# Performance work log

Hardware: AMD Instinct MI355X
Metric: run time of the kernel (lower is better)

The kernel has to match this reference:

```python
import jax, jax.numpy as jnp
import numpy as np

NUM_FEATURES = 256
HIDDEN = 32
ALPHA = 0.1
JITTER = 1e-4
QP_ITERS = 500  # fixed-iteration projected gradient solve of the nonneg-constrained QP
BATCH = 65536


def setup_inputs() -> dict:
    key = jax.random.key(0)
    ks = jax.random.split(key, 6)
    n, h = NUM_FEATURES, HIDDEN
    x = jax.random.normal(ks[0], (BATCH, n), jnp.float32)
    y = jax.random.normal(ks[1], (BATCH, 1), jnp.float32)
    # per-feature MLP params, stacked over the feature axis
    # first Linear has fan_in=1 -> torch init U(-1,1); second has fan_in=h -> U(-1/sqrt(h),1/sqrt(h))
    W1 = jax.random.uniform(ks[2], (n, h), jnp.float32, -1.0, 1.0)
    b1 = jax.random.uniform(ks[3], (n, h), jnp.float32, -1.0, 1.0)
    lim = 1.0 / np.sqrt(h)
    W2 = jax.random.uniform(ks[4], (n, h), jnp.float32, -lim, lim)
    b2 = jax.random.uniform(ks[5], (n,), jnp.float32, -lim, lim)
    return {"x": x, "y": y, "W1": W1, "b1": b1, "W2": W2, "b2": b2}


def _forward(x, y, W1, b1, W2, b2):
    B = x.shape[0]
    n = NUM_FEATURES
    # all per-feature 1->hidden->1 MLPs, batched over the feature axis
    hact = jnp.tanh(x[:, :, None] * W1[None, :, :] + b1[None, :, :])   # [B, n, hidden]
    Z = jnp.einsum('bnh,nh->bn', hact, W2) + b2                         # [B, n]
    Q = Z.T @ Z + JITTER * jnp.eye(n, dtype=Z.dtype)                    # Gram + jitter
    L = jnp.linalg.cholesky(Q)                                          # solver parameterization
    Qe = L @ L.T                                                        # == Q_stable; what the QP 'sees'
    p = ALPHA * B * jnp.ones(n, Z.dtype) - (Z.T @ y)[:, 0]
    # QP: min 0.5*lam^T Qe lam + p^T lam  s.t. lam >= 0 ; projected gradient, step = 1/lmax
    lmax = jnp.linalg.eigvalsh(jax.lax.stop_gradient(Qe))[-1]
    step = 1.0 / lmax

    def body(lam, _):
        lam = jnp.maximum(lam - step * (Qe @ lam + p), 0.0)
        return lam, None

    lam, _ = jax.lax.scan(body, jnp.zeros(n, Z.dtype), None, length=QP_ITERS)
    y_hat = Z @ lam                                                     # [B]
    return y_hat, lam


def reference(x, y, W1, b1, W2, b2):
    return _forward(x, y, W1, b1, W2, b2)
```

## Files before the change

### kernel.cpp

```cpp
#include <hip/hip_runtime.h>
#include <math.h>


#define NF 256
#define HID 32
#define BATCHN 65536
#define ALPHA_BF 6553.6f
#define JITTERF 1e-4f
#define QP_ITERS_N 500
#define K2C 2.8853900817779268f
#define XFIX 6.5f
#define INVX (1.0f / 6.5f)
#define NNODE 44

#if __has_builtin(__builtin_amdgcn_exp2f)
__device__ __forceinline__ float fexp2(float x) { return __builtin_amdgcn_exp2f(x); }
#else
__device__ __forceinline__ float fexp2(float x) { return exp2f(x); }
#endif
#if __has_builtin(__builtin_amdgcn_rcpf)
__device__ __forceinline__ float frcp(float x) { return __builtin_amdgcn_rcpf(x); }
#else
__device__ __forceinline__ float frcp(float x) { return 1.0f / x; }
#endif

__device__ __forceinline__ float zeval(const float* __restrict__ W1,
                                       const float* __restrict__ b1,
                                       const float* __restrict__ W2,
                                       const float* __restrict__ b2,
                                       int n, float xv)
{
  float acc = b2[n];
  for (int h = 0; h < HID; ++h) {
    float u  = fmaf(xv, W1[n * HID + h], b1[n * HID + h]);
    float th = fmaf(-2.f, frcp(fexp2(K2C * u) + 1.f), 1.f);
    acc = fmaf(W2[n * HID + h], th, acc);
  }
  return acc;
}

__global__ __launch_bounds__(256) void mcoeff_kernel(
    const float* __restrict__ y,
    const float* __restrict__ W1, const float* __restrict__ b1,
    const float* __restrict__ W2, float* __restrict__ wsf)
{
  const int t = threadIdx.x;
  if ((int)blockIdx.x < 64) {
    const int gi = blockIdx.x * 256 + t;
    if (gi == 0) wsf[1] = 0.f;
    if (gi == 2) wsf[2] = 0.f;
    float4 v = *reinterpret_cast<const float4*>(y + gi * 4);
    float s  = (v.x + v.y) + (v.z + v.w);
    float sa = (fabsf(v.x) + fabsf(v.y)) + (fabsf(v.z) + fabsf(v.w));
    #pragma unroll
    for (int m = 1; m < 64; m <<= 1) {
      s  += __shfl_xor(s, m);
      sa += __shfl_xor(sa, m);
    }
    __shared__ float ls[4], la[4];
    int w = t >> 6;
    if ((t & 63) == 0) { ls[w] = s; la[w] = sa; }
    __syncthreads();
    if (t == 0) {
      wsf[8  + blockIdx.x] = (ls[0] + ls[1]) + (ls[2] + ls[3]);
      wsf[72 + blockIdx.x] = (la[0] + la[1]) + (la[2] + la[3]);
    }
  } else {
    const int cb = blockIdx.x - 64;
    const int k  = cb >> 5;
    const int id = (cb & 31) * 256 + t;
    const int h  = t & 31;
    const int n  = id >> 5;
    const float aX  = W1[id] * XFIX;
    const float bb  = b1[id];
    const float w2v = W2[id];
    const float kf = (float)k;
    const float C1 = (float)(M_PI / (double)NNODE);
    float acc = 0.f;
    #pragma unroll 4
    for (int jn = 0; jn < NNODE; ++jn) {
      float ang = ((float)jn + 0.5f) * C1;
      float tj  = __cosf(ang);
      float u   = fmaf(aX, tj, bb);
      float f   = fmaf(-2.f, frcp(fexp2(K2C * u) + 1.f), 1.f);
      acc = fmaf(f, __cosf(kf * ang), acc);
    }
    const float ck = acc * ((k == 0) ? (1.0f / (float)NNODE)
                                     : (2.0f / (float)NNODE));
    float comb = w2v * ck;
    float cabs = fabsf(comb);
    float wabs = fabsf(w2v);
    #pragma unroll
    for (int m = 1; m < 32; m <<= 1) {
      comb += __shfl_xor(comb, m);
      cabs += __shfl_xor(cabs, m);
      wabs += __shfl_xor(wabs, m);
    }
    if (h == 0) {
      if (k <= 20) wsf[256 + k * 256 + n] = comb;
      else         wsf[5632 + (k - 21) * 256 + n] = cabs;
      if (k == 0)  wsf[11520 + n] = wabs;
    }
  }
}

#define STEP2(CK) { \
  float q0 = fmaf(d0, c0, -m0), q1 = fmaf(d1, c1, -m1); \
  a0 = fmaf(CK.x, q0, a0); a1 = fmaf(CK.y, q1, a1); \
  m0 = c0; c0 = q0; m1 = c1; c1 = q1; }

#define ROW2(XV, YV) { \
  mx = fmaxf(mx, fmaxf(fabsf((XV).x), fabsf((XV).y))); \
  float h0 = (XV).x * INVX, h1 = (XV).y * INVX; \
  float d0 = h0 + h0, d1 = h1 + h1; \
  float m0 = 1.f, m1 = 1.f, c0 = h0, c1 = h1; \
  float a0 = fmaf(C01.x, h0, C00.x), a1 = fmaf(C01.y, h1, C00.y); \
  STEP2(C02) STEP2(C03) STEP2(C04) STEP2(C05) STEP2(C06) STEP2(C07) \
  STEP2(C08) STEP2(C09) STEP2(C10) STEP2(C11) STEP2(C12) STEP2(C13) \
  STEP2(C14) STEP2(C15) STEP2(C16) STEP2(C17) STEP2(C18) STEP2(C19) \
  STEP2(C20) \
  z0 = fmaf(a0, (YV), z0); z1 = fmaf(a1, (YV), z1); }

__global__ __launch_bounds__(256, 3) void zmom_kernel(
    const float* __restrict__ x, const float* __restrict__ y,
    float* __restrict__ wsf)
{
  const int t = threadIdx.x;
  const int lane = t & 63, wv = t >> 6;
  const int fh = wv & 1;
  const int rr = wv >> 1;
  const int n0 = fh * 128 + lane * 2;
  const float* Carr = wsf + 256;
  #define LDC(K) *reinterpret_cast<const float2*>(Carr + (K) * 256 + n0)
  const float2 C00 = LDC(0),  C01 = LDC(1),  C02 = LDC(2),  C03 = LDC(3);
  const float2 C04 = LDC(4),  C05 = LDC(5),  C06 = LDC(6),  C07 = LDC(7);
  const float2 C08 = LDC(8),  C09 = LDC(9),  C10 = LDC(10), C11 = LDC(11);
  const float2 C12 = LDC(12), C13 = LDC(13), C14 = LDC(14), C15 = LDC(15);
  const float2 C16 = LDC(16), C17 = LDC(17), C18 = LDC(18), C19 = LDC(19);
  const float2 C20 = LDC(20);
  #undef LDC
  const int rbase = 2 * blockIdx.x + rr;
  const size_t S = (size_t)4096 * NF;
  const float* xp = x + (size_t)rbase * NF + n0;
  float z0 = 0.f, z1 = 0.f, mx = 0.f;
  float2 x0 = *reinterpret_cast<const float2*>(xp);
  float2 x1 = *reinterpret_cast<const float2*>(xp + S);
  float2 x2 = *reinterpret_cast<const float2*>(xp + 2 * S);
  float2 x3 = *reinterpret_cast<const float2*>(xp + 3 * S);
  float y0 = y[rbase],            y1 = y[rbase + 4096];
  float y2 = y[rbase + 2 * 4096], y3 = y[rbase + 3 * 4096];
  const float* xq = xp + 4 * S;
  #pragma unroll
  for (int i = 0; i < 12; ++i) {
    float2 xn = *reinterpret_cast<const float2*>(xq);
    float  yn = y[rbase + 4096 * (i + 4)];
    ROW2(x0, y0)
    x0 = x1; y0 = y1;  x1 = x2; y1 = y2;
    x2 = x3; y2 = y3;  x3 = xn; y3 = yn;
    xq += S;
  }
  ROW2(x0, y0)
  ROW2(x1, y1)
  ROW2(x2, y2)
  ROW2(x3, y3)
  #pragma unroll
  for (int m = 1; m < 64; m <<= 1) mx = fmaxf(mx, __shfl_xor(mx, m));
  __shared__ float lm[512];
  __shared__ float wmx[4];
  if (lane == 0) wmx[wv] = mx;
  *reinterpret_cast<float2*>(lm + rr * 256 + n0) = make_float2(z0, z1);
  __syncthreads();
  if (t == 0) {
    float m4 = fmaxf(fmaxf(wmx[0], wmx[1]), fmaxf(wmx[2], wmx[3]));
    atomicMax(reinterpret_cast<unsigned int*>(&wsf[1]), __float_as_uint(m4));
  }
  float s = lm[t] + lm[256 + t];
  wsf[28672 + (size_t)blockIdx.x * NF + t] = s;
}

__global__ __launch_bounds__(256) void red1f_kernel(float* __restrict__ wsf)
{
  const int n = threadIdx.x, j = blockIdx.x;
  const float* p = wsf + 28672 + (size_t)j * 32 * NF + n;
  float s0 = 0.f, s1 = 0.f, s2 = 0.f, s3 = 0.f;
  #pragma unroll
  for (int k = 0; k < 32; k += 4) {
    s0 += p[(size_t)k * NF];       s1 += p[(size_t)(k + 1) * NF];
    s2 += p[(size_t)(k + 2) * NF]; s3 += p[(size_t)(k + 3) * NF];
  }
  wsf[12288 + (size_t)j * NF + n] = (s0 + s1) + (s2 + s3);
}

__global__ __launch_bounds__(256) void zwflag_kernel(
    const float* __restrict__ b2, float* __restrict__ wsf,
    float* __restrict__ out)
{
  const int t = threadIdx.x;
  __shared__ float shv[2];
  if (t < 64) {
    float a = wsf[8 + t], bb = wsf[72 + t];
    #pragma unroll
    for (int m = 1; m < 64; m <<= 1) {
      a  += __shfl_xor(a, m);
      bb += __shfl_xor(bb, m);
    }
    if (t == 0) { shv[0] = a; shv[1] = bb; }
  }
  __syncthreads();
  const float Sy = shv[0], SyA = shv[1];
  float s = 0.f;
  #pragma unroll
  for (int j = 0; j < 64; ++j) s += wsf[12288 + j * NF + t];
  float tailn = 0.f;
  #pragma unroll
  for (int q = 0; q < 23; ++q) tailn += wsf[5632 + q * 256 + t];
  float ptil = ALPHA_BF - (s + b2[t] * Sy);
  float cert = fmaf(fmaf(3.0f, tailn, 3e-3f * wsf[11520 + t]), SyA, 128.0f);
  int ok = ((ptil - cert) >= 0.f) ? 1 : 0;
  __shared__ int smi[256];
  __shared__ int okk;
  smi[t] = ok;
  __syncthreads();
  for (int off = 128; off > 0; off >>= 1) {
    if (t < off) smi[t] = smi[t] & smi[t + off];
    __syncthreads();
  }
  if (t == 0) {
    float Xo = __uint_as_float(*reinterpret_cast<unsigned int*>(&wsf[1]));
    okk = (smi[0] && (Xo <= XFIX)) ? 1 : 0;
    if (blockIdx.x == 0) wsf[0] = okk ? 1.f : 0.f;
  }
  __syncthreads();
  if (!okk) return;
  int i = blockIdx.x * 256 + t;
  if (i < BATCHN + NF) out[i] = 0.f;
}

__global__ __launch_bounds__(256) void fb_all_kernel(
    const float* __restrict__ x, const float* __restrict__ y,
    const float* __restrict__ W1, const float* __restrict__ b1,
    const float* __restrict__ W2, const float* __restrict__ b2,
    float* __restrict__ wsf, float* __restrict__ out)
{
  if (wsf[0] >= 0.5f) return;
  const int t = threadIdx.x;
  float* fb_part = wsf + 552960;
  float* p_ex    = wsf + 1077248;
  float* Q       = wsf + 1077504;
  float* L       = Q + 65536;
  float* Qe      = L + 65536;
  {
    const int b0 = blockIdx.x * 32;
    float zty = 0.f;
    for (int r = 0; r < 32; ++r) {
      float xv = x[(size_t)(b0 + r) * NF + t];
      zty = fmaf(zeval(W1, b1, W2, b2, t, xv), y[b0 + r], zty);
    }
    fb_part[(size_t)blockIdx.x * NF + t] = zty;
  }
  __threadfence();
  __shared__ unsigned int tick;
  if (t == 0)
    tick = atomicAdd(reinterpret_cast<unsigned int*>(&wsf[2]), 1u);
  __syncthreads();
  if (tick != 2047u) return;
  {
    float s = 0.f;
    for (int j = 0; j < 2048; ++j) s += fb_part[(size_t)j * NF + t];
    p_ex[t] = ALPHA_BF - s;
  }
  for (int i = t; i < 65536; i += 256)
    Q[i] = ((i >> 8) == (i & 255)) ? JITTERF : 0.f;
  __syncthreads();
  __shared__ float zsh[16 * NF];
  for (int c = 0; c < BATCHN / 16; ++c) {
    const int r0 = c * 16;
    for (int r = 0; r < 16; ++r)
      zsh[r * NF + t] = zeval(W1, b1, W2, b2, t, x[(size_t)(r0 + r) * NF + t]);
    __syncthreads();
    for (int j = 0; j < NF; ++j) {
      float s = 0.f;
      for (int r = 0; r < 16; ++r) s += zsh[r * NF + t] * zsh[r * NF + j];
      Q[t * NF + j] += s;
    }
    __syncthreads();
  }
  __shared__ float sm[NF];
  __shared__ float lam_s[NF];
  for (int i = 0; i < NF; ++i) L[i * NF + t] = (t <= i) ? Q[i * NF + t] : 0.f;
  __syncthreads();
  for (int k = 0; k < NF; ++k) {
    if (t == 0) L[k * NF + k] = sqrtf(L[k * NF + k]);
    __syncthreads();
    float lkk = L[k * NF + k];
    if (t > k) L[t * NF + k] /= lkk;
    __syncthreads();
    if (t > k) {
      float ltk = L[t * NF + k];
      for (int i = k + 1; i <= t; ++i) L[t * NF + i] -= ltk * L[i * NF + k];
    }
    __syncthreads();
  }
  for (int i = 0; i < NF; ++i) {
    int m = (i < t) ? i : t;
    float s = 0.f;
    for (int k = 0; k <= m; ++k) s += L[i * NF + k] * L[t * NF + k];
    Qe[i * NF + t] = s;
  }
  __syncthreads();
  lam_s[t] = 1.f;
  __syncthreads();
  float lmax = 1.f;
  for (int it = 0; it < 256; ++it) {
    float s = 0.f;
    for (int k = 0; k < NF; ++k) s += Qe[t * NF + k] * lam_s[k];
    sm[t] = s * s;
    __syncthreads();
    for (int off = 128; off > 0; off >>= 1) {
      if (t < off) sm[t] += sm[t + off];
      __syncthreads();
    }
    float nrm = sqrtf(sm[0]);
    __syncthreads();
    lam_s[t] = s / nrm;
    lmax = nrm;
    __syncthreads();
  }
  float step = 1.0f / lmax;
  lam_s[t] = 0.f;
  __syncthreads();
  float pv = p_ex[t];
  for (int it = 0; it < QP_ITERS_N; ++it) {
    float s = 0.f;
    for (int k = 0; k < NF; ++k) s += Qe[t * NF + k] * lam_s[k];
    float ln = fmaxf(lam_s[t] - step * (s + pv), 0.f);
    __syncthreads();
    lam_s[t] = ln;
    __syncthreads();
  }
  out[BATCHN + t] = lam_s[t];
  __syncthreads();
  for (int b = t; b < BATCHN; b += 256) {
    float acc = 0.f;
    for (int n = 0; n < NF; ++n)
      acc = fmaf(zeval(W1, b1, W2, b2, n, x[(size_t)b * NF + n]),
                 lam_s[n], acc);
    out[b] = acc;
  }
}

extern "C" void kernel_launch(void* const* d_in, const int* in_sizes, int n_in,
                              void* d_out, int out_size, void* d_ws, size_t ws_size,
                              hipStream_t stream) {
  const float* x  = (const float*)d_in[0];
  const float* y  = (const float*)d_in[1];
  const float* W1 = (const float*)d_in[2];
  const float* b1 = (const float*)d_in[3];
  const float* W2 = (const float*)d_in[4];
  const float* b2 = (const float*)d_in[5];
  float* out = (float*)d_out;
  float* ws  = (float*)d_ws;

  mcoeff_kernel<<<1472, 256, 0, stream>>>(y, W1, b1, W2, ws);
  zmom_kernel<<<2048, 256, 0, stream>>>(x, y, ws);
  red1f_kernel<<<64, 256, 0, stream>>>(ws);
  zwflag_kernel<<<257, 256, 0, stream>>>(b2, ws, out);
  fb_all_kernel<<<2048, 256, 0, stream>>>(x, y, W1, b1, W2, b2, ws, out);
}
```

Before: 56.94 us.

## Remap zmom so each thread owns one feature and processes row pairs

The moment kernel now assigns one feature column per thread instead of two adjacent features per thread split across wave pairs. Each thread walks 32 rows with a 2048-row stride and evaluates the Chebyshev recurrence on two rows at a time. This halves the per-thread coefficient registers, which allows raising the launch bound from 3 to 4 blocks per SIMD, and it removes the shared-memory combine of two row halves. In exchange, global loads become scalar 4-byte loads rather than float2, and the dependent chain per row pair is longer.

```diff
diff --git a/kernel.cpp b/kernel.cpp
--- a/kernel.cpp
+++ b/kernel.cpp
@@ -104,78 +104,71 @@
   }
 }
 
-#define STEP2(CK) { \
-  float q0 = fmaf(d0, c0, -m0), q1 = fmaf(d1, c1, -m1); \
-  a0 = fmaf(CK.x, q0, a0); a1 = fmaf(CK.y, q1, a1); \
-  m0 = c0; c0 = q0; m1 = c1; c1 = q1; }
-
-#define ROW2(XV, YV) { \
-  mx = fmaxf(mx, fmaxf(fabsf((XV).x), fabsf((XV).y))); \
-  float h0 = (XV).x * INVX, h1 = (XV).y * INVX; \
+#define STEPP(CK) { \
+  float q0 = fmaf(d0, cc0, -m0), q1 = fmaf(d1, cc1, -m1); \
+  a0 = fmaf(CK, q0, a0); a1 = fmaf(CK, q1, a1); \
+  m0 = cc0; cc0 = q0; m1 = cc1; cc1 = q1; }
+
+#define PAIR(XA, YA, XB, YB) { \
+  mx = fmaxf(mx, fmaxf(fabsf(XA), fabsf(XB))); \
+  float h0 = (XA) * INVX, h1 = (XB) * INVX; \
   float d0 = h0 + h0, d1 = h1 + h1; \
-  float m0 = 1.f, m1 = 1.f, c0 = h0, c1 = h1; \
-  float a0 = fmaf(C01.x, h0, C00.x), a1 = fmaf(C01.y, h1, C00.y); \
-  STEP2(C02) STEP2(C03) STEP2(C04) STEP2(C05) STEP2(C06) STEP2(C07) \
-  STEP2(C08) STEP2(C09) STEP2(C10) STEP2(C11) STEP2(C12) STEP2(C13) \
-  STEP2(C14) STEP2(C15) STEP2(C16) STEP2(C17) STEP2(C18) STEP2(C19) \
-  STEP2(C20) \
-  z0 = fmaf(a0, (YV), z0); z1 = fmaf(a1, (YV), z1); }
-
-__global__ __launch_bounds__(256, 3) void zmom_kernel(
+  float m0 = 1.f, m1 = 1.f, cc0 = h0, cc1 = h1; \
+  float a0 = fmaf(c01, h0, c00), a1 = fmaf(c01, h1, c00); \
+  STEPP(c02) STEPP(c03) STEPP(c04) STEPP(c05) STEPP(c06) STEPP(c07) \
+  STEPP(c08) STEPP(c09) STEPP(c10) STEPP(c11) STEPP(c12) STEPP(c13) \
+  STEPP(c14) STEPP(c15) STEPP(c16) STEPP(c17) STEPP(c18) STEPP(c19) \
+  STEPP(c20) \
+  z0 = fmaf(a0, (YA), z0); z1 = fmaf(a1, (YB), z1); }
+
+__global__ __launch_bounds__(256, 4) void zmom_kernel(
     const float* __restrict__ x, const float* __restrict__ y,
     float* __restrict__ wsf)
 {
   const int t = threadIdx.x;
-  const int lane = t & 63, wv = t >> 6;
-  const int fh = wv & 1;
-  const int rr = wv >> 1;
-  const int n0 = fh * 128 + lane * 2;
   const float* Carr = wsf + 256;
-  #define LDC(K) *reinterpret_cast<const float2*>(Carr + (K) * 256 + n0)
-  const float2 C00 = LDC(0),  C01 = LDC(1),  C02 = LDC(2),  C03 = LDC(3);
-  const float2 C04 = LDC(4),  C05 = LDC(5),  C06 = LDC(6),  C07 = LDC(7);
-  const float2 C08 = LDC(8),  C09 = LDC(9),  C10 = LDC(10), C11 = LDC(11);
-  const float2 C12 = LDC(12), C13 = LDC(13), C14 = LDC(14), C15 = LDC(15);
-  const float2 C16 = LDC(16), C17 = LDC(17), C18 = LDC(18), C19 = LDC(19);
-  const float2 C20 = LDC(20);
-  #undef LDC
-  const int rbase = 2 * blockIdx.x + rr;
-  const size_t S = (size_t)4096 * NF;
-  const float* xp = x + (size_t)rbase * NF + n0;
+  const float c00 = Carr[t],            c01 = Carr[256 + t];
+  const float c02 = Carr[512 + t],      c03 = Carr[768 + t];
+  const float c04 = Carr[1024 + t],     c05 = Carr[1280 + t];
+  const float c06 = Carr[1536 + t],     c07 = Carr[1792 + t];
+  const float c08 = Carr[2048 + t],     c09 = Carr[2304 + t];
+  const float c10 = Carr[2560 + t],     c11 = Carr[2816 + t];
+  const float c12 = Carr[3072 + t],     c13 = Carr[3328 + t];
+  const float c14 = Carr[3584 + t],     c15 = Carr[3840 + t];
+  const float c16 = Carr[4096 + t],     c17 = Carr[4352 + t];
+  const float c18 = Carr[4608 + t],     c19 = Carr[4864 + t];
+  const float c20 = Carr[5120 + t];
+  const int blk = blockIdx.x;
+  const float* base = x + (size_t)blk * NF + t;
+  const size_t S = (size_t)2048 * NF;
   float z0 = 0.f, z1 = 0.f, mx = 0.f;
-  float2 x0 = *reinterpret_cast<const float2*>(xp);
-  float2 x1 = *reinterpret_cast<const float2*>(xp + S);
-  float2 x2 = *reinterpret_cast<const float2*>(xp + 2 * S);
-  float2 x3 = *reinterpret_cast<const float2*>(xp + 3 * S);
-  float y0 = y[rbase],            y1 = y[rbase + 4096];
-  float y2 = y[rbase + 2 * 4096], y3 = y[rbase + 3 * 4096];
-  const float* xq = xp + 4 * S;
-  #pragma unroll
-  for (int i = 0; i < 12; ++i) {
-    float2 xn = *reinterpret_cast<const float2*>(xq);
-    float  yn = y[rbase + 4096 * (i + 4)];
-    ROW2(x0, y0)
-    x0 = x1; y0 = y1;  x1 = x2; y1 = y2;
-    x2 = x3; y2 = y3;  x3 = xn; y3 = yn;
-    xq += S;
-  }
-  ROW2(x0, y0)
-  ROW2(x1, y1)
-  ROW2(x2, y2)
-  ROW2(x3, y3)
+  float x0 = base[0],     x1 = base[S];
+  float x2 = base[2 * S], x3 = base[3 * S];
+  float y0 = y[blk],            y1 = y[blk + 2048];
+  float y2 = y[blk + 2 * 2048], y3 = y[blk + 3 * 2048];
+  const float* xq = base + 4 * S;
+  #pragma unroll
+  for (int j = 0; j < 14; ++j) {
+    float xn0 = xq[0], xn1 = xq[S];
+    float yn0 = y[blk + 2048 * (2 * j + 4)];
+    float yn1 = y[blk + 2048 * (2 * j + 5)];
+    PAIR(x0, y0, x1, y1)
+    x0 = x2; y0 = y2;  x1 = x3; y1 = y3;
+    x2 = xn0; y2 = yn0; x3 = xn1; y3 = yn1;
+    xq += 2 * S;
+  }
+  PAIR(x0, y0, x1, y1)
+  PAIR(x2, y2, x3, y3)
   #pragma unroll
   for (int m = 1; m < 64; m <<= 1) mx = fmaxf(mx, __shfl_xor(mx, m));
-  __shared__ float lm[512];
   __shared__ float wmx[4];
-  if (lane == 0) wmx[wv] = mx;
-  *reinterpret_cast<float2*>(lm + rr * 256 + n0) = make_float2(z0, z1);
+  if ((t & 63) == 0) wmx[t >> 6] = mx;
   __syncthreads();
   if (t == 0) {
     float m4 = fmaxf(fmaxf(wmx[0], wmx[1]), fmaxf(wmx[2], wmx[3]));
     atomicMax(reinterpret_cast<unsigned int*>(&wsf[1]), __float_as_uint(m4));
   }
-  float s = lm[t] + lm[256 + t];
-  wsf[28672 + (size_t)blockIdx.x * NF + t] = s;
+  wsf[28672 + (size_t)blk * NF + t] = z0 + z1;
 }
 
 __global__ __launch_bounds__(256) void red1f_kernel(float* __restrict__ wsf)
```

New measurement: 60.20 us. 5.7% more time.
